# Performance work log

Hardware: AMD Instinct MI355X
Metric: run time of the kernel (lower is better)

## Reference

```python
import jax, jax.numpy as jnp
import numpy as np

D_EMB = 256
SCALE = 0.02
B, T = 4, 4096
EPS = 1e-5


def layer_norm(x, w, b):
    m = jnp.mean(x, axis=-1, keepdims=True)
    v = jnp.mean((x - m) ** 2, axis=-1, keepdims=True)
    return (x - m) * jax.lax.rsqrt(v + EPS) * w + b


def setup_inputs() -> dict:
    key = jax.random.key(0)
    ks = jax.random.split(key, 4)
    x = jax.random.normal(ks[0], (B, T, D_EMB), dtype=jnp.float32)
    qkv = jax.random.normal(ks[1], (3, D_EMB, D_EMB), dtype=jnp.float32) * SCALE
    # nn.Linear(D, 2D, bias=False): weight shape (2D, D), applied as x @ W.T
    w1 = jax.random.normal(ks[2], (2 * D_EMB, D_EMB), dtype=jnp.float32) * (1.0 / np.sqrt(D_EMB))
    w2 = jax.random.normal(ks[3], (D_EMB, 2 * D_EMB), dtype=jnp.float32) * (1.0 / np.sqrt(2 * D_EMB))
    ones = jnp.ones((D_EMB,), dtype=jnp.float32)
    zeros = jnp.zeros((D_EMB,), dtype=jnp.float32)
    return {
        "x": x, "qkv": qkv,
        "ln_q_w": ones, "ln_q_b": zeros,
        "ln_k_w": ones, "ln_k_b": zeros,
        "ln_attn_w": ones, "ln_attn_b": zeros,
        "w1": w1, "w2": w2,
        "ln_ff_w": ones, "ln_ff_b": zeros,
    }


def reference(x, qkv, ln_q_w, ln_q_b, ln_k_w, ln_k_b, ln_attn_w, ln_attn_b, w1, w2, ln_ff_w, ln_ff_b):
    # QKV projections: [3, B, T, D]
    y = jnp.einsum('btd,ndD->nbtD', x, qkv)
    q, k, v = y[0], y[1], y[2]
    q = layer_norm(q, ln_q_w, ln_q_b)
    k = layer_norm(k, ln_k_w, ln_k_b)
    # full (non-causal) single-head attention, scale by sqrt(D_EMB)
    scores = jnp.einsum('btd,bsd->bts', q, k) / jnp.sqrt(jnp.float32(D_EMB))
    attn = jax.nn.softmax(scores, axis=-1)
    y = jnp.einsum('bts,bsd->btd', attn, v)
    y = layer_norm(y, ln_attn_w, ln_attn_b)
    x = 0.7 * (x + y)
    # FFN with dual leaky_relu
    y = jax.nn.leaky_relu(x @ w1.T, negative_slope=0.2)
    y = jax.nn.leaky_relu(y @ w2.T, negative_slope=0.2)
    y = layer_norm(y, ln_ff_w, ln_ff_b)
    return 0.7 * (x + y)
```

## Files before the change

kernel.cpp:

```cpp
#include <hip/hip_runtime.h>

#define BSZ   4
#define TSEQ  4096
#define DEMB  256
#define NTOK  (BSZ * TSEQ)
#define HID   512
#define SPLITS 4
#define KEYS_PER_SPLIT (TSEQ / SPLITS)
#define TK 32
#define NT (KEYS_PER_SPLIT / TK)
#define KIMG_STRIDE 8704
#define VIMG_STRIDE 10240

using bf16x8 = __attribute__((ext_vector_type(8))) short;
using f32x16 = __attribute__((ext_vector_type(16))) float;

static __device__ __forceinline__ unsigned short f2bf(float f) {
  union { float f; unsigned u; } v; v.f = f;
  unsigned r = v.u + 0x7FFF + ((v.u >> 16) & 1);
  return (unsigned short)(r >> 16);
}
static __device__ __forceinline__ float bf2f(unsigned short u) {
  union { unsigned u; float f; } v; v.u = ((unsigned)u) << 16;
  return v.f;
}

static __device__ __forceinline__ void async16(void* lds, const void* gp) {
  __builtin_amdgcn_global_load_lds(
      (const __attribute__((address_space(1))) unsigned int*)gp,
      (__attribute__((address_space(3))) unsigned int*)lds, 16, 0, 0);
}

static __device__ __forceinline__ void plswap(unsigned& a, unsigned& b) {
  using uint2v = __attribute__((ext_vector_type(2))) unsigned int;
  uint2v r = __builtin_amdgcn_permlane32_swap(a, b, false, false);
  a = r[0]; b = r[1];
}

__global__ __launch_bounds__(256) void prep_kernel(
    const float* __restrict__ qkv, const float* __restrict__ w1,
    const float* __restrict__ w2, unsigned short* __restrict__ qkvT,
    unsigned short* __restrict__ w1b, unsigned short* __restrict__ w2b)
{
  const int tid = threadIdx.x;
  if (blockIdx.y < 3) {
    if (blockIdx.x >= 16) return;
    __shared__ float Ts[64][65];
    const int z  = blockIdx.y;
    const int k0 = (blockIdx.x >> 2) * 64;
    const int j0 = (blockIdx.x & 3) * 64;
    const float* src = qkv + (size_t)z * DEMB * DEMB + (size_t)k0 * DEMB + j0;
#pragma unroll
    for (int p = 0; p < 4; ++p) {
      int idx = p * 256 + tid;
      int r = idx >> 4, g = idx & 15;
      float4 v = *(const float4*)(src + (size_t)r * DEMB + g * 4);
      Ts[r][g * 4 + 0] = v.x; Ts[r][g * 4 + 1] = v.y;
      Ts[r][g * 4 + 2] = v.z; Ts[r][g * 4 + 3] = v.w;
    }
    __syncthreads();
    unsigned short* dst = qkvT + (size_t)z * DEMB * DEMB + (size_t)j0 * DEMB + k0;
#pragma unroll
    for (int p = 0; p < 4; ++p) {
      int idx = p * 256 + tid;
      int r = idx >> 4, g = idx & 15;
      ushort4 o;
      o.x = f2bf(Ts[g * 4 + 0][r]); o.y = f2bf(Ts[g * 4 + 1][r]);
      o.z = f2bf(Ts[g * 4 + 2][r]); o.w = f2bf(Ts[g * 4 + 3][r]);
      *(ushort4*)(dst + (size_t)r * DEMB + g * 4) = o;
    }
  } else {
    const float* s = (blockIdx.y == 3) ? w1 : w2;
    unsigned short* d = (blockIdx.y == 3) ? w1b : w2b;
    const int i = blockIdx.x * 256 + tid;
    float4 v = ((const float4*)s)[i];
    ushort4 o;
    o.x = f2bf(v.x); o.y = f2bf(v.y); o.z = f2bf(v.z); o.w = f2bf(v.w);
    ((ushort4*)d)[i] = o;
  }
}

__global__ __launch_bounds__(512, 1) void qkvln_kernel(
    const float* __restrict__ x, const unsigned short* __restrict__ qkvT,
    const float* __restrict__ lnqw, const float* __restrict__ lnqb,
    const float* __restrict__ lnkw, const float* __restrict__ lnkb,
    unsigned short* __restrict__ Qbn, unsigned short* __restrict__ Kimg,
    unsigned short* __restrict__ Vimg)
{
  __shared__ __align__(16) unsigned short sh[36864];
  unsigned short* As = sh;
  unsigned short* Bs = sh + 256 * 72;

  const int tid = threadIdx.x;
  const int w   = tid >> 6;
  const int l   = tid & 63;
  const int lm  = l & 31;
  const int lh  = l >> 5;
  const int z   = blockIdx.y;
  const int m0  = blockIdx.x * 256;
  const int bb  = m0 >> 12;

  const unsigned short* Bt = qkvT + (size_t)z * DEMB * DEMB;

  f32x16 o[8];
#pragma unroll
  for (int t = 0; t < 8; ++t)
#pragma unroll
    for (int r = 0; r < 16; ++r) o[t][r] = 0.f;

  const int fr = tid >> 4;
  const int fc = (tid & 15) * 4;

  float4 arf[8];
  bf16x8 brb[4];

#pragma unroll
  for (int i = 0; i < 8; ++i)
    arf[i] = *(const float4*)(x + (size_t)(m0 + fr + 32 * i) * DEMB + fc);
#pragma unroll
  for (int i = 0; i < 4; ++i) {
    const int c = tid + 512 * i;
    brb[i] = *(const bf16x8*)(Bt + (size_t)(c >> 3) * DEMB + (c & 7) * 8);
  }

  for (int k0 = 0; k0 < DEMB; k0 += 64) {
    __syncthreads();
#pragma unroll
    for (int i = 0; i < 8; ++i) {
      ushort4 u;
      u.x = f2bf(arf[i].x); u.y = f2bf(arf[i].y);
      u.z = f2bf(arf[i].z); u.w = f2bf(arf[i].w);
      *(ushort4*)&As[(fr + 32 * i) * 72 + fc] = u;
    }
#pragma unroll
    for (int i = 0; i < 4; ++i) {
      const int c = tid + 512 * i;
      *(bf16x8*)&Bs[(c >> 3) * 72 + (c & 7) * 8] = brb[i];
    }
    __syncthreads();

    if (k0 + 64 < DEMB) {
      const int kn = k0 + 64;
#pragma unroll
      for (int i = 0; i < 8; ++i)
        arf[i] = *(const float4*)(x + (size_t)(m0 + fr + 32 * i) * DEMB + kn + fc);
#pragma unroll
      for (int i = 0; i < 4; ++i) {
        const int c = tid + 512 * i;
        brb[i] = *(const bf16x8*)(Bt + (size_t)(c >> 3) * DEMB + kn + (c & 7) * 8);
      }
    }

#pragma unroll
    for (int ks = 0; ks < 4; ++ks) {
      bf16x8 a = *(const bf16x8*)&As[(w * 32 + lm) * 72 + ks * 16 + lh * 8];
#pragma unroll
      for (int t = 0; t < 8; ++t) {
        bf16x8 b = *(const bf16x8*)&Bs[(t * 32 + lm) * 72 + ks * 16 + lh * 8];
        o[t] = __builtin_amdgcn_mfma_f32_32x32x16_bf16(a, b, o[t], 0, 0, 0);
      }
    }
  }

  __syncthreads();

  if (z < 2) {
    const float* wp = z ? lnkw : lnqw;
    const float* bp = z ? lnkb : lnqb;
    float wc[8], bc[8];
#pragma unroll
    for (int t = 0; t < 8; ++t) { wc[t] = wp[t * 32 + lm]; bc[t] = bp[t * 32 + lm]; }
#pragma unroll
    for (int r = 0; r < 16; ++r) {
      float sv = 0.f, sq = 0.f;
#pragma unroll
      for (int t = 0; t < 8; ++t) { const float v = o[t][r]; sv += v; sq += v * v; }
#pragma unroll
      for (int d = 1; d < 32; d <<= 1) { sv += __shfl_xor(sv, d, 64); sq += __shfl_xor(sq, d, 64); }
      const float mean = sv * (1.f / DEMB);
      const float rs = rsqrtf(sq * (1.f / DEMB) - mean * mean + 1e-5f);
      const int token = m0 + w * 32 + (r & 3) + 8 * (r >> 2) + 4 * lh;
      if (z == 0) {
        unsigned short* dst = Qbn + (size_t)token * DEMB;
#pragma unroll
        for (int t = 0; t < 8; ++t)
          dst[t * 32 + lm] = f2bf((o[t][r] - mean) * rs * wc[t] + bc[t]);
      } else {
        const int t5 = token & 4095;
        unsigned short* dst =
            Kimg + (size_t)(bb * 128 + (t5 >> 5)) * KIMG_STRIDE + (t5 & 31) * 264;
#pragma unroll
        for (int t = 0; t < 8; ++t)
          dst[t * 32 + lm] = f2bf((o[t][r] - mean) * rs * wc[t] + bc[t]);
      }
    }
  } else {
#pragma unroll
    for (int h = 0; h < 2; ++h) {
      if (h) __syncthreads();
#pragma unroll
      for (int t2 = 0; t2 < 4; ++t2) {
        const int t = h * 4 + t2;
#pragma unroll
        for (int r = 0; r < 16; ++r) {
          const int row = w * 32 + (r & 3) + 8 * (r >> 2) + 4 * lh;
          sh[row * 130 + t2 * 32 + lm] = f2bf(o[t][r]);
        }
      }
      __syncthreads();
      const int d2 = tid & 127;
      const int tq = tid >> 7;
      const int d  = h * 128 + d2;
#pragma unroll
      for (int j = 0; j < 16; ++j) {
        const int tok0 = tq * 64 + j * 4;
        ushort4 v;
        v.x = sh[(tok0 + 0) * 130 + d2];
        v.y = sh[(tok0 + 1) * 130 + d2];
        v.z = sh[(tok0 + 2) * 130 + d2];
        v.w = sh[(tok0 + 3) * 130 + d2];
        const int gtok = m0 + tok0;
        const int kt = (gtok & 4095) >> 5;
        *(ushort4*)(Vimg + (size_t)(bb * 128 + kt) * VIMG_STRIDE + d * 40 + (tok0 & 31)) = v;
      }
    }
  }
}

__global__ __launch_bounds__(256, 3) void gemm_ffn_kernel(
    const unsigned short* __restrict__ A, const unsigned short* __restrict__ Bt,
    unsigned short* __restrict__ C, int M, int N, int K)
{
  __shared__ __align__(16) unsigned short As[128 * 72];
  __shared__ __align__(16) unsigned short Bs[128 * 72];

  const int tid = threadIdx.x;
  const int w   = tid >> 6;
  const int wm  = w >> 1, wn = w & 1;
  const int l   = tid & 63;
  const int lm  = l & 31;
  const int lh  = l >> 5;

  const int m0    = blockIdx.x * 128;
  const int nbase = blockIdx.y * 128;

  f32x16 acc00, acc01, acc10, acc11;
#pragma unroll
  for (int r = 0; r < 16; ++r) { acc00[r] = 0.f; acc01[r] = 0.f; acc10[r] = 0.f; acc11[r] = 0.f; }

  const int lr = tid >> 3;
  const int lc = (tid & 7) * 8;

  bf16x8 arb[4], brb[4];

#pragma unroll
  for (int i = 0; i < 4; ++i) {
    arb[i] = *(const bf16x8*)(A  + (size_t)(m0 + i * 32 + lr) * K + lc);
    brb[i] = *(const bf16x8*)(Bt + (size_t)(nbase + i * 32 + lr) * K + lc);
  }

  for (int k0 = 0; k0 < K; k0 += 64) {
    __syncthreads();
#pragma unroll
    for (int i = 0; i < 4; ++i) {
      *(bf16x8*)&As[(i * 32 + lr) * 72 + lc] = arb[i];
      *(bf16x8*)&Bs[(i * 32 + lr) * 72 + lc] = brb[i];
    }
    __syncthreads();

    if (k0 + 64 < K) {
      const int kn = k0 + 64;
#pragma unroll
      for (int i = 0; i < 4; ++i) {
        arb[i] = *(const bf16x8*)(A  + (size_t)(m0 + i * 32 + lr) * K + kn + lc);
        brb[i] = *(const bf16x8*)(Bt + (size_t)(nbase + i * 32 + lr) * K + kn + lc);
      }
    }

#pragma unroll
    for (int ks = 0; ks < 4; ++ks) {
      bf16x8 a0 = *(const bf16x8*)&As[(wm * 64 + lm)      * 72 + ks * 16 + lh * 8];
      bf16x8 a1 = *(const bf16x8*)&As[(wm * 64 + 32 + lm) * 72 + ks * 16 + lh * 8];
      bf16x8 b0 = *(const bf16x8*)&Bs[(wn * 64 + lm)      * 72 + ks * 16 + lh * 8];
      bf16x8 b1 = *(const bf16x8*)&Bs[(wn * 64 + 32 + lm) * 72 + ks * 16 + lh * 8];
      acc00 = __builtin_amdgcn_mfma_f32_32x32x16_bf16(a0, b0, acc00, 0, 0, 0);
      acc01 = __builtin_amdgcn_mfma_f32_32x32x16_bf16(a0, b1, acc01, 0, 0, 0);
      acc10 = __builtin_amdgcn_mfma_f32_32x32x16_bf16(a1, b0, acc10, 0, 0, 0);
      acc11 = __builtin_amdgcn_mfma_f32_32x32x16_bf16(a1, b1, acc11, 0, 0, 0);
    }
  }

  const f32x16* accs[4] = { &acc00, &acc01, &acc10, &acc11 };
#pragma unroll
  for (int am = 0; am < 2; ++am)
#pragma unroll
    for (int bn = 0; bn < 2; ++bn) {
      const f32x16& a = *accs[am * 2 + bn];
#pragma unroll
      for (int r = 0; r < 16; ++r) {
        const int m = m0 + wm * 64 + am * 32 + (r & 3) + 8 * (r >> 2) + 4 * lh;
        const int n = nbase + wn * 64 + bn * 32 + lm;
        float v = a[r];
        v = v > 0.f ? v : 0.2f * v;
        C[(size_t)m * N + n] = f2bf(v);
      }
    }
}

__global__ __launch_bounds__(256) void ln_res_bf16_kernel(
    const unsigned short* __restrict__ Y, const float* __restrict__ Xin,
    const float* __restrict__ w, const float* __restrict__ b,
    float* __restrict__ Out)
{
  const int lane = threadIdx.x & 63;
  const size_t row = (size_t)blockIdx.x * 4 + (threadIdx.x >> 6);
  ushort4 u = *(const ushort4*)&Y[row * DEMB + lane * 4];
  float y0 = bf2f(u.x), y1 = bf2f(u.y), y2 = bf2f(u.z), y3 = bf2f(u.w);
  float s  = y0 + y1 + y2 + y3;
  float sq = y0 * y0 + y1 * y1 + y2 * y2 + y3 * y3;
#pragma unroll
  for (int o = 32; o > 0; o >>= 1) { s += __shfl_down(s, o); sq += __shfl_down(sq, o); }
  s = __shfl(s, 0); sq = __shfl(sq, 0);
  const float m  = s * (1.f / DEMB);
  const float rs = rsqrtf(sq * (1.f / DEMB) - m * m + 1e-5f);
  const float4 wv = *(const float4*)&w[lane * 4];
  const float4 bv = *(const float4*)&b[lane * 4];
  const float4 xi = *(const float4*)&Xin[row * DEMB + lane * 4];
  float4 o;
  o.x = 0.7f * (xi.x + (y0 - m) * rs * wv.x + bv.x);
  o.y = 0.7f * (xi.y + (y1 - m) * rs * wv.y + bv.y);
  o.z = 0.7f * (xi.z + (y2 - m) * rs * wv.z + bv.z);
  o.w = 0.7f * (xi.w + (y3 - m) * rs * wv.w + bv.w);
  *(float4*)&Out[row * DEMB + lane * 4] = o;
}

__global__ __launch_bounds__(256, 2) void attn_split_kernel(
    const unsigned short* __restrict__ Qb, const unsigned short* __restrict__ Kimg,
    const unsigned short* __restrict__ Vimg, unsigned short* __restrict__ Opart,
    float* __restrict__ lpart)
{
  __shared__ __align__(16) unsigned short Ks[2][KIMG_STRIDE];
  __shared__ __align__(16) unsigned short Vs[2][VIMG_STRIDE];

  const int tid = threadIdx.x;
  const int w   = tid >> 6;
  const int l   = tid & 63;
  const int lm  = l & 31;
  const int lh  = l >> 5;

  const int lin = blockIdx.x;
  const int xcd = lin & 7;
  const int idx = lin >> 3;
  const int b     = xcd >> 1;
  const int split = (xcd & 1) * 2 + (idx & 1);
  const int q0    = (idx >> 1) * 128;

  const unsigned short* Qbase  = Qb + (size_t)b * TSEQ * DEMB;
  const unsigned short* Ktiles = Kimg + (size_t)(b * 128 + split * 32) * KIMG_STRIDE;
  const unsigned short* Vtiles = Vimg + (size_t)(b * 128 + split * 32) * VIMG_STRIDE;

  bf16x8 qf[16];
  {
    const unsigned short* qrow = Qbase + (size_t)(q0 + w * 32 + lm) * DEMB + lh * 8;
#pragma unroll
    for (int ks = 0; ks < 16; ++ks) qf[ks] = *(const bf16x8*)(qrow + ks * 16);
  }

  f32x16 o[8];
#pragma unroll
  for (int t = 0; t < 8; ++t)
#pragma unroll
    for (int r = 0; r < 16; ++r) o[t][r] = 0.f;
  float psum = 0.f;

  bf16x8 pva, pvb;

  auto DMAK = [&](int t, int buf) {
    const unsigned short* kp = Ktiles + (size_t)t * KIMG_STRIDE;
#pragma unroll
    for (int i = 0; i < 5; ++i) {
      const int c = w + 4 * i;
      if (c < 17) async16(&Ks[buf][c * 512], kp + c * 512 + l * 8);
    }
  };
  auto DMAV = [&](int t, int buf) {
    const unsigned short* vp = Vtiles + (size_t)t * VIMG_STRIDE;
#pragma unroll
    for (int i = 0; i < 5; ++i) {
      const int c = w + 4 * i;
      async16(&Vs[buf][c * 512], vp + c * 512 + l * 8);
    }
  };
  auto QK = [&](int buf) {
    f32x16 s;
#pragma unroll
    for (int r = 0; r < 16; ++r) s[r] = 0.f;
    const unsigned short* Kp = &Ks[buf][0];
#pragma unroll
    for (int ks = 0; ks < 16; ++ks) {
      bf16x8 kf = *(const bf16x8*)&Kp[lm * 264 + ks * 16 + lh * 8];
      s = __builtin_amdgcn_mfma_f32_32x32x16_bf16(kf, qf[ks], s, 0, 0, 0);
    }
    return s;
  };
  auto PV = [&](int buf) {
    const unsigned short* Vp = &Vs[buf][0];
#pragma unroll
    for (int t = 0; t < 8; ++t) {
      bf16x8 vf0 = *(const bf16x8*)&Vp[(t * 32 + lm) * 40 + lh * 8];
      o[t] = __builtin_amdgcn_mfma_f32_32x32x16_bf16(pva, vf0, o[t], 0, 0, 0);
      bf16x8 vf1 = *(const bf16x8*)&Vp[(t * 32 + lm) * 40 + 16 + lh * 8];
      o[t] = __builtin_amdgcn_mfma_f32_32x32x16_bf16(pvb, vf1, o[t], 0, 0, 0);
    }
  };
  auto SM = [&](const f32x16& s) {
    float e[16];
#pragma unroll
    for (int i = 0; i < 16; ++i)
      e[i] = exp2f(s[i] * 0.09016844335f - 11.541560327f);
    const float t0 = (e[0] + e[1]) + (e[2] + e[3]);
    const float t1 = (e[4] + e[5]) + (e[6] + e[7]);
    const float t2 = (e[8] + e[9]) + (e[10] + e[11]);
    const float t3 = (e[12] + e[13]) + (e[14] + e[15]);
    psum += (t0 + t1) + (t2 + t3);
    unsigned pk[8];
#pragma unroll
    for (int i = 0; i < 8; ++i)
      asm("v_cvt_pk_bf16_f32 %0, %1, %2" : "=v"(pk[i]) : "v"(e[2 * i]), "v"(e[2 * i + 1]));
    plswap(pk[0], pk[2]);
    plswap(pk[1], pk[3]);
    plswap(pk[4], pk[6]);
    plswap(pk[5], pk[7]);
    union U8 { unsigned u[4]; bf16x8 v; } A, B;
    A.u[0] = pk[0]; A.u[1] = pk[1]; A.u[2] = pk[2]; A.u[3] = pk[3];
    B.u[0] = pk[4]; B.u[1] = pk[5]; B.u[2] = pk[6]; B.u[3] = pk[7];
    pva = A.v; pvb = B.v;
  };

  DMAK(0, 0); DMAV(0, 0);
  __syncthreads();
  DMAK(1, 1);
  f32x16 s = QK(0);
  __syncthreads();
  DMAV(1, 1);
  SM(s);

  for (int j = 1; j < NT; ++j) {
    const int kc = j & 1, kn = kc ^ 1;
    if (j + 1 < NT) DMAK(j + 1, kn);
    const unsigned short* Kp = &Ks[kc][0];
    const unsigned short* Vp = &Vs[kn][0];
    f32x16 sn;
#pragma unroll
    for (int r = 0; r < 16; ++r) sn[r] = 0.f;
    __builtin_amdgcn_s_setprio(1);
#pragma unroll
    for (int i = 0; i < 16; ++i) {
      bf16x8 kf = *(const bf16x8*)&Kp[lm * 264 + i * 16 + lh * 8];
      sn = __builtin_amdgcn_mfma_f32_32x32x16_bf16(kf, qf[i], sn, 0, 0, 0);
      if (i < 8) {
        bf16x8 vf = *(const bf16x8*)&Vp[(i * 32 + lm) * 40 + lh * 8];
        o[i] = __builtin_amdgcn_mfma_f32_32x32x16_bf16(pva, vf, o[i], 0, 0, 0);
      } else {
        bf16x8 vf = *(const bf16x8*)&Vp[((i - 8) * 32 + lm) * 40 + 16 + lh * 8];
        o[i - 8] = __builtin_amdgcn_mfma_f32_32x32x16_bf16(pvb, vf, o[i - 8], 0, 0, 0);
      }
    }
    __builtin_amdgcn_s_setprio(0);
    s = sn;
    __syncthreads();
    if (j + 1 < NT) DMAV(j + 1, kn);
    SM(s);
  }

  PV((NT - 1) & 1);

  const float tot = psum + __shfl_xor(psum, 32, 64);

  unsigned short* Ob =
      Opart + ((size_t)split * NTOK + (size_t)b * TSEQ + q0 + w * 32) * DEMB;
  float* lb = lpart + (size_t)split * NTOK + (size_t)b * TSEQ + q0 + w * 32;
#pragma unroll
  for (int r = 0; r < 16; ++r) {
    const int row = (r & 3) + ((r >> 2) << 3) + (lh << 2);
#pragma unroll
    for (int t = 0; t < 8; ++t)
      Ob[(size_t)row * DEMB + t * 32 + lm] = f2bf(o[t][r]);
  }
  if (lh == 0) lb[lm] = tot;
}

__global__ __launch_bounds__(256) void combine_lnres_kernel(
    const unsigned short* __restrict__ Opart, const float* __restrict__ lpart,
    const float* __restrict__ Xin, const float* __restrict__ w,
    const float* __restrict__ b, float* __restrict__ Out,
    unsigned short* __restrict__ Outb)
{
  const int lane = threadIdx.x & 63;
  const size_t row = (size_t)blockIdx.x * 4 + (threadIdx.x >> 6);
  float4 acc = make_float4(0.f, 0.f, 0.f, 0.f);
  float lt = 0.f;
#pragma unroll
  for (int p = 0; p < SPLITS; ++p) {
    const ushort4 u = *(const ushort4*)&Opart[((size_t)p * NTOK + row) * DEMB + lane * 4];
    acc.x += bf2f(u.x); acc.y += bf2f(u.y);
    acc.z += bf2f(u.z); acc.w += bf2f(u.w);
    lt += lpart[(size_t)p * NTOK + row];
  }
  const float inv = 1.f / lt;
  const float y0 = acc.x * inv, y1 = acc.y * inv, y2 = acc.z * inv, y3 = acc.w * inv;
  float s  = y0 + y1 + y2 + y3;
  float sq = y0 * y0 + y1 * y1 + y2 * y2 + y3 * y3;
#pragma unroll
  for (int o = 32; o > 0; o >>= 1) { s += __shfl_down(s, o); sq += __shfl_down(sq, o); }
  s = __shfl(s, 0); sq = __shfl(sq, 0);
  const float m  = s * (1.f / DEMB);
  const float rs = rsqrtf(sq * (1.f / DEMB) - m * m + 1e-5f);
  const float4 wv = *(const float4*)&w[lane * 4];
  const float4 bv = *(const float4*)&b[lane * 4];
  const float4 xi = *(const float4*)&Xin[row * DEMB + lane * 4];
  float4 o;
  o.x = 0.7f * (xi.x + (y0 - m) * rs * wv.x + bv.x);
  o.y = 0.7f * (xi.y + (y1 - m) * rs * wv.y + bv.y);
  o.z = 0.7f * (xi.z + (y2 - m) * rs * wv.z + bv.z);
  o.w = 0.7f * (xi.w + (y3 - m) * rs * wv.w + bv.w);
  *(float4*)&Out[row * DEMB + lane * 4] = o;
  ushort4 ob;
  ob.x = f2bf(o.x); ob.y = f2bf(o.y); ob.z = f2bf(o.z); ob.w = f2bf(o.w);
  *(ushort4*)&Outb[row * DEMB + lane * 4] = ob;
}

extern "C" void kernel_launch(void* const* d_in, const int* in_sizes, int n_in,
                              void* d_out, int out_size, void* d_ws, size_t ws_size,
                              hipStream_t stream)
{
  (void)in_sizes; (void)n_in; (void)out_size; (void)ws_size;
  const float* x    = (const float*)d_in[0];
  const float* qkv  = (const float*)d_in[1];
  const float* lnqw = (const float*)d_in[2];
  const float* lnqb = (const float*)d_in[3];
  const float* lnkw = (const float*)d_in[4];
  const float* lnkb = (const float*)d_in[5];
  const float* lnaw = (const float*)d_in[6];
  const float* lnab = (const float*)d_in[7];
  const float* w1   = (const float*)d_in[8];
  const float* w2   = (const float*)d_in[9];
  const float* lnfw = (const float*)d_in[10];
  const float* lnfb = (const float*)d_in[11];
  float* out = (float*)d_out;

  char* W = (char*)d_ws;
  const size_t MB = 1 << 20;
  unsigned short* Qbn   = (unsigned short*)(W + 0);
  unsigned short* Kimg  = (unsigned short*)(W + 8 * MB);
  unsigned short* Vimg  = (unsigned short*)(W + 17 * MB);
  unsigned short* Opart = (unsigned short*)(W + 28 * MB);
  float*          lpart = (float*)(W + 60 * MB);
  unsigned short* x1b   = (unsigned short*)(W + 0);
  unsigned short* H     = (unsigned short*)(W + 8 * MB);
  unsigned short* Y2b   = (unsigned short*)(W + 28 * MB);
  unsigned short* qkvT  = (unsigned short*)(W + 60 * MB + 512 * 1024);
  unsigned short* w1b   = (unsigned short*)(W + 61 * MB);
  unsigned short* w2b   = (unsigned short*)(W + 61 * MB + 256 * 1024);

  const dim3 blk(256);

  prep_kernel<<<dim3(128, 5), blk, 0, stream>>>(qkv, w1, w2, qkvT, w1b, w2b);

  qkvln_kernel<<<dim3(NTOK / 256, 3), dim3(512), 0, stream>>>(
      x, qkvT, lnqw, lnqb, lnkw, lnkb, Qbn, Kimg, Vimg);

  attn_split_kernel<<<dim3(512), dim3(256), 0, stream>>>(Qbn, Kimg, Vimg, Opart, lpart);
  combine_lnres_kernel<<<NTOK / 4, blk, 0, stream>>>(Opart, lpart, x, lnaw, lnab, out, x1b);

  gemm_ffn_kernel<<<dim3(NTOK / 128, HID / 128), blk, 0, stream>>>(
      x1b, w1b, H, NTOK, HID, DEMB);
  gemm_ffn_kernel<<<dim3(NTOK / 128, DEMB / 128), blk, 0, stream>>>(
      H, w2b, Y2b, NTOK, DEMB, HID);

  ln_res_bf16_kernel<<<NTOK / 4, blk, 0, stream>>>(Y2b, out, lnfw, lnfb, out);
}
```

Measured before the change: 216.2 us.

## Use 512-thread attention blocks with triple-buffered K/V async pipeline

```diff
diff --git a/kernel.cpp b/kernel.cpp
--- a/kernel.cpp
+++ b/kernel.cpp
@@ -334,13 +334,13 @@
   *(float4*)&Out[row * DEMB + lane * 4] = o;
 }
 
-__global__ __launch_bounds__(256, 2) void attn_split_kernel(
+__global__ __launch_bounds__(512, 1) void attn_split_kernel(
     const unsigned short* __restrict__ Qb, const unsigned short* __restrict__ Kimg,
     const unsigned short* __restrict__ Vimg, unsigned short* __restrict__ Opart,
     float* __restrict__ lpart)
 {
-  __shared__ __align__(16) unsigned short Ks[2][KIMG_STRIDE];
-  __shared__ __align__(16) unsigned short Vs[2][VIMG_STRIDE];
+  __shared__ __align__(16) unsigned short Ks[3][12288];
+  __shared__ __align__(16) unsigned short Vs[3][12288];
 
   const int tid = threadIdx.x;
   const int w   = tid >> 6;
@@ -353,7 +353,7 @@
   const int idx = lin >> 3;
   const int b     = xcd >> 1;
   const int split = (xcd & 1) * 2 + (idx & 1);
-  const int q0    = (idx >> 1) * 128;
+  const int q0    = (idx >> 1) * 256;
 
   const unsigned short* Qbase  = Qb + (size_t)b * TSEQ * DEMB;
   const unsigned short* Ktiles = Kimg + (size_t)(b * 128 + split * 32) * KIMG_STRIDE;
@@ -376,32 +376,24 @@
   bf16x8 pva, pvb;
 
   auto DMAK = [&](int t, int buf) {
-    const unsigned short* kp = Ktiles + (size_t)t * KIMG_STRIDE;
-#pragma unroll
-    for (int i = 0; i < 5; ++i) {
-      const int c = w + 4 * i;
-      if (c < 17) async16(&Ks[buf][c * 512], kp + c * 512 + l * 8);
+    const int tc = t < NT ? t : NT - 1;
+    const unsigned short* kp = Ktiles + (size_t)tc * KIMG_STRIDE;
+#pragma unroll
+    for (int i = 0; i < 3; ++i) {
+      const int c  = w + 8 * i;
+      const int ck = c < 17 ? c : 0;
+      async16(&Ks[buf][c * 512], kp + ck * 512 + l * 8);
     }
   };
   auto DMAV = [&](int t, int buf) {
-    const unsigned short* vp = Vtiles + (size_t)t * VIMG_STRIDE;
-#pragma unroll
-    for (int i = 0; i < 5; ++i) {
-      const int c = w + 4 * i;
-      async16(&Vs[buf][c * 512], vp + c * 512 + l * 8);
-    }
-  };
-  auto QK = [&](int buf) {
-    f32x16 s;
-#pragma unroll
-    for (int r = 0; r < 16; ++r) s[r] = 0.f;
-    const unsigned short* Kp = &Ks[buf][0];
-#pragma unroll
-    for (int ks = 0; ks < 16; ++ks) {
-      bf16x8 kf = *(const bf16x8*)&Kp[lm * 264 + ks * 16 + lh * 8];
-      s = __builtin_amdgcn_mfma_f32_32x32x16_bf16(kf, qf[ks], s, 0, 0, 0);
-    }
-    return s;
+    const int tc = t < NT ? t : NT - 1;
+    const unsigned short* vp = Vtiles + (size_t)tc * VIMG_STRIDE;
+#pragma unroll
+    for (int i = 0; i < 3; ++i) {
+      const int c  = w + 8 * i;
+      const int cv = c < 20 ? c : 0;
+      async16(&Vs[buf][c * 512], vp + cv * 512 + l * 8);
+    }
   };
   auto PV = [&](int buf) {
     const unsigned short* Vp = &Vs[buf][0];
@@ -437,19 +429,38 @@
     pva = A.v; pvb = B.v;
   };
 
-  DMAK(0, 0); DMAV(0, 0);
-  __syncthreads();
-  DMAK(1, 1);
-  f32x16 s = QK(0);
-  __syncthreads();
-  DMAV(1, 1);
+  DMAK(0, 0); DMAK(1, 1); DMAV(0, 0);
+
+  asm volatile("s_waitcnt vmcnt(6)" ::: "memory");
+  __builtin_amdgcn_s_barrier();
+  DMAK(2, 2); DMAV(1, 1);
+  f32x16 s;
+  {
+    f32x16 sn;
+#pragma unroll
+    for (int r = 0; r < 16; ++r) sn[r] = 0.f;
+    const unsigned short* Kp = &Ks[0][0];
+#pragma unroll
+    for (int i = 0; i < 16; ++i) {
+      bf16x8 kf = *(const bf16x8*)&Kp[lm * 264 + i * 16 + lh * 8];
+      sn = __builtin_amdgcn_mfma_f32_32x32x16_bf16(kf, qf[i], sn, 0, 0, 0);
+    }
+    s = sn;
+  }
   SM(s);
 
+  int kc = 1;
   for (int j = 1; j < NT; ++j) {
-    const int kc = j & 1, kn = kc ^ 1;
-    if (j + 1 < NT) DMAK(j + 1, kn);
+    asm volatile("s_waitcnt vmcnt(6)" ::: "memory");
+    __builtin_amdgcn_s_barrier();
+
+    const int kb = (kc == 0) ? 2 : kc - 1;
+    const int vb = (kc == 2) ? 0 : kc + 1;
+    DMAK(j + 2, kb);
+    DMAV(j + 1, vb);
+
     const unsigned short* Kp = &Ks[kc][0];
-    const unsigned short* Vp = &Vs[kn][0];
+    const unsigned short* Vp = &Vs[kb][0];
     f32x16 sn;
 #pragma unroll
     for (int r = 0; r < 16; ++r) sn[r] = 0.f;
@@ -468,12 +479,14 @@
     }
     __builtin_amdgcn_s_setprio(0);
     s = sn;
-    __syncthreads();
-    if (j + 1 < NT) DMAV(j + 1, kn);
     SM(s);
-  }
-
-  PV((NT - 1) & 1);
+
+    kc = (kc == 2) ? 0 : kc + 1;
+  }
+
+  asm volatile("s_waitcnt vmcnt(0)" ::: "memory");
+  __builtin_amdgcn_s_barrier();
+  PV((NT - 1) % 3);
 
   const float tot = psum + __shfl_xor(psum, 32, 64);
 
@@ -570,7 +583,7 @@
   qkvln_kernel<<<dim3(NTOK / 256, 3), dim3(512), 0, stream>>>(
       x, qkvT, lnqw, lnqb, lnkw, lnkb, Qbn, Kimg, Vimg);
 
-  attn_split_kernel<<<dim3(512), dim3(256), 0, stream>>>(Qbn, Kimg, Vimg, Opart, lpart);
+  attn_split_kernel<<<dim3(256), dim3(512), 0, stream>>>(Qbn, Kimg, Vimg, Opart, lpart);
   combine_lnres_kernel<<<NTOK / 4, blk, 0, stream>>>(Opart, lpart, x, lnaw, lnab, out, x1b);
 
   gemm_ffn_kernel<<<dim3(NTOK / 128, HID / 128), blk, 0, stream>>>(
```

Measured after the change: 220.2 us. No clear change (+1.9%).

## Fuse second FFN GEMM with leaky ReLU, LayerNorm and residual epilogue

Applied to the files above, without the earlier changes.

```diff
diff --git a/kernel.cpp b/kernel.cpp
--- a/kernel.cpp
+++ b/kernel.cpp
@@ -307,31 +307,96 @@
     }
 }
 
-__global__ __launch_bounds__(256) void ln_res_bf16_kernel(
-    const unsigned short* __restrict__ Y, const float* __restrict__ Xin,
-    const float* __restrict__ w, const float* __restrict__ b,
-    float* __restrict__ Out)
+__global__ __launch_bounds__(256, 2) void gemm2_lnres_kernel(
+    const unsigned short* __restrict__ A,
+    const unsigned short* __restrict__ Bt,
+    const float* __restrict__ lw, const float* __restrict__ lb,
+    float* __restrict__ X1out)
 {
-  const int lane = threadIdx.x & 63;
-  const size_t row = (size_t)blockIdx.x * 4 + (threadIdx.x >> 6);
-  ushort4 u = *(const ushort4*)&Y[row * DEMB + lane * 4];
-  float y0 = bf2f(u.x), y1 = bf2f(u.y), y2 = bf2f(u.z), y3 = bf2f(u.w);
-  float s  = y0 + y1 + y2 + y3;
-  float sq = y0 * y0 + y1 * y1 + y2 * y2 + y3 * y3;
-#pragma unroll
-  for (int o = 32; o > 0; o >>= 1) { s += __shfl_down(s, o); sq += __shfl_down(sq, o); }
-  s = __shfl(s, 0); sq = __shfl(sq, 0);
-  const float m  = s * (1.f / DEMB);
-  const float rs = rsqrtf(sq * (1.f / DEMB) - m * m + 1e-5f);
-  const float4 wv = *(const float4*)&w[lane * 4];
-  const float4 bv = *(const float4*)&b[lane * 4];
-  const float4 xi = *(const float4*)&Xin[row * DEMB + lane * 4];
-  float4 o;
-  o.x = 0.7f * (xi.x + (y0 - m) * rs * wv.x + bv.x);
-  o.y = 0.7f * (xi.y + (y1 - m) * rs * wv.y + bv.y);
-  o.z = 0.7f * (xi.z + (y2 - m) * rs * wv.z + bv.z);
-  o.w = 0.7f * (xi.w + (y3 - m) * rs * wv.w + bv.w);
-  *(float4*)&Out[row * DEMB + lane * 4] = o;
+  __shared__ __align__(16) unsigned short As[128 * 72];
+  __shared__ __align__(16) unsigned short Bs[256 * 72];
+
+  const int tid = threadIdx.x;
+  const int w   = tid >> 6;
+  const int l   = tid & 63;
+  const int lm  = l & 31;
+  const int lh  = l >> 5;
+  const int m0  = blockIdx.x * 128;
+
+  f32x16 o[8];
+#pragma unroll
+  for (int t = 0; t < 8; ++t)
+#pragma unroll
+    for (int r = 0; r < 16; ++r) o[t][r] = 0.f;
+
+  const int lr = tid >> 3;
+  const int lc = (tid & 7) * 8;
+
+  bf16x8 arb[4], brb[8];
+
+#pragma unroll
+  for (int i = 0; i < 4; ++i)
+    arb[i] = *(const bf16x8*)(A + (size_t)(m0 + i * 32 + lr) * HID + lc);
+#pragma unroll
+  for (int i = 0; i < 8; ++i)
+    brb[i] = *(const bf16x8*)(Bt + (size_t)(i * 32 + lr) * HID + lc);
+
+  for (int k0 = 0; k0 < HID; k0 += 64) {
+    __syncthreads();
+#pragma unroll
+    for (int i = 0; i < 4; ++i)
+      *(bf16x8*)&As[(i * 32 + lr) * 72 + lc] = arb[i];
+#pragma unroll
+    for (int i = 0; i < 8; ++i)
+      *(bf16x8*)&Bs[(i * 32 + lr) * 72 + lc] = brb[i];
+    __syncthreads();
+
+    if (k0 + 64 < HID) {
+      const int kn = k0 + 64;
+#pragma unroll
+      for (int i = 0; i < 4; ++i)
+        arb[i] = *(const bf16x8*)(A + (size_t)(m0 + i * 32 + lr) * HID + kn + lc);
+#pragma unroll
+      for (int i = 0; i < 8; ++i)
+        brb[i] = *(const bf16x8*)(Bt + (size_t)(i * 32 + lr) * HID + kn + lc);
+    }
+
+#pragma unroll
+    for (int ks = 0; ks < 4; ++ks) {
+      bf16x8 a = *(const bf16x8*)&As[(w * 32 + lm) * 72 + ks * 16 + lh * 8];
+#pragma unroll
+      for (int t = 0; t < 8; ++t) {
+        bf16x8 b = *(const bf16x8*)&Bs[(t * 32 + lm) * 72 + ks * 16 + lh * 8];
+        o[t] = __builtin_amdgcn_mfma_f32_32x32x16_bf16(a, b, o[t], 0, 0, 0);
+      }
+    }
+  }
+
+  float wc[8], bc[8];
+#pragma unroll
+  for (int t = 0; t < 8; ++t) { wc[t] = lw[t * 32 + lm]; bc[t] = lb[t * 32 + lm]; }
+#pragma unroll
+  for (int r = 0; r < 16; ++r) {
+    float sv = 0.f, sq = 0.f;
+#pragma unroll
+    for (int t = 0; t < 8; ++t) {
+      float v = o[t][r];
+      v = v > 0.f ? v : 0.2f * v;
+      o[t][r] = v;
+      sv += v; sq += v * v;
+    }
+#pragma unroll
+    for (int d = 1; d < 32; d <<= 1) { sv += __shfl_xor(sv, d, 64); sq += __shfl_xor(sq, d, 64); }
+    const float mean = sv * (1.f / DEMB);
+    const float rs = rsqrtf(sq * (1.f / DEMB) - mean * mean + 1e-5f);
+    const int token = m0 + w * 32 + (r & 3) + 8 * (r >> 2) + 4 * lh;
+    float* rowp = X1out + (size_t)token * DEMB;
+#pragma unroll
+    for (int t = 0; t < 8; ++t) {
+      const float xi = rowp[t * 32 + lm];
+      rowp[t * 32 + lm] = 0.7f * (xi + (o[t][r] - mean) * rs * wc[t] + bc[t]);
+    }
+  }
 }
 
 __global__ __launch_bounds__(256, 2) void attn_split_kernel(
@@ -558,7 +623,6 @@
   float*          lpart = (float*)(W + 60 * MB);
   unsigned short* x1b   = (unsigned short*)(W + 0);
   unsigned short* H     = (unsigned short*)(W + 8 * MB);
-  unsigned short* Y2b   = (unsigned short*)(W + 28 * MB);
   unsigned short* qkvT  = (unsigned short*)(W + 60 * MB + 512 * 1024);
   unsigned short* w1b   = (unsigned short*)(W + 61 * MB);
   unsigned short* w2b   = (unsigned short*)(W + 61 * MB + 256 * 1024);
@@ -575,8 +639,6 @@
 
   gemm_ffn_kernel<<<dim3(NTOK / 128, HID / 128), blk, 0, stream>>>(
       x1b, w1b, H, NTOK, HID, DEMB);
-  gemm_ffn_kernel<<<dim3(NTOK / 128, DEMB / 128), blk, 0, stream>>>(
-      H, w2b, Y2b, NTOK, DEMB, HID);
-
-  ln_res_bf16_kernel<<<NTOK / 4, blk, 0, stream>>>(Y2b, out, lnfw, lnfb, out);
-}
+  gemm2_lnres_kernel<<<dim3(NTOK / 128), blk, 0, stream>>>(
+      H, w2b, lnfw, lnfb, out);
+}
```

Measured after the change: 221.8 us. +2.6%, slower.
